# Optimization experiments

Hardware: AMD Instinct MI355X
Metric: run time of the kernel (lower is better)

## Reference

```python
import jax, jax.numpy as jnp
import numpy as np

N = 8192
IN_F = 512
OUT_F = 256

def setup_inputs() -> dict:
    key = jax.random.key(0)
    k1, k2, k3 = jax.random.split(key, 3)
    A = jax.random.uniform(k1, (N, N), dtype=jnp.float32)
    X = jax.random.normal(k2, (N, IN_F), dtype=jnp.float32)
    init_range = np.sqrt(6.0 / (IN_F + OUT_F)).astype(np.float32)
    W = jax.random.uniform(k3, (IN_F, OUT_F), dtype=jnp.float32,
                           minval=-init_range, maxval=init_range)
    return {"weighted_adjacency_matrix": A, "feature_matrix": X, "weight": W}

def reference(weighted_adjacency_matrix, feature_matrix, weight):
    A = weighted_adjacency_matrix
    # d = (1 + row_sum(A))^{-1/2}; D^{-1/2} A D^{-1/2} via row/col broadcast scaling
    d = jax.lax.rsqrt(1.0 + jnp.sum(A, axis=1))            # [N]
    norm_adj = d[:, None] * A * d[None, :]                  # [N, N]
    support = feature_matrix @ weight                       # [N, out_features]
    return norm_adj @ support                               # [N, out_features]
```

## Files before the change

### kernel.cpp

```cpp
#include <hip/hip_runtime.h>
#include <hip/hip_bf16.h>
#include <stdint.h>

#define NROW 8192
#define INF  512
#define OUTF 256

typedef __attribute__((ext_vector_type(8))) short bf16x8;
typedef __attribute__((ext_vector_type(4))) float f32x4;

__device__ __forceinline__ unsigned short f2bf(float x) {
  union { float f; unsigned u; } v; v.f = x;
  unsigned r = v.u + 0x7fffu + ((v.u >> 16) & 1u);
  return (unsigned short)(r >> 16);
}
__device__ __forceinline__ unsigned short f2bf_fast(float x) {
  union { float f; unsigned u; } v; v.f = x;
  return (unsigned short)((v.u + 0x8000u) >> 16);
}
__device__ __forceinline__ float bf2f(unsigned short h) {
  union { unsigned u; float f; } v; v.u = ((unsigned)h) << 16;
  return v.f;
}

__device__ __forceinline__ void async_cp16(const void* g, void* l) {
  __builtin_amdgcn_global_load_lds((const __attribute__((address_space(1))) void*)g,
                                   (__attribute__((address_space(3))) void*)l,
                                   16, 0, 0);
}

__global__ __launch_bounds__(256) void k_rowsum_convert(
    const float* __restrict__ A, unsigned short* __restrict__ Ab,
    float* __restrict__ dv) {
  int w = threadIdx.x >> 6, lane = threadIdx.x & 63;
  int row = blockIdx.x * 4 + w;
  const float4* ar = (const float4*)(A + (size_t)row * NROW);
  ushort4* br = (ushort4*)(Ab + (size_t)row * NROW);
  float s = 0.f;
  #pragma unroll 4
  for (int it = 0; it < NROW / 256; ++it) {
    float4 v = ar[it * 64 + lane];
    s += (v.x + v.y) + (v.z + v.w);
    ushort4 b;
    b.x = f2bf_fast(v.x); b.y = f2bf_fast(v.y);
    b.z = f2bf_fast(v.z); b.w = f2bf_fast(v.w);
    br[it * 64 + lane] = b;
  }
  #pragma unroll
  for (int off = 32; off > 0; off >>= 1) s += __shfl_down(s, off, 64);
  if (lane == 0) dv[row] = rsqrtf(1.f + s);
}

__global__ __launch_bounds__(256) void k_convert_w(
    const float* __restrict__ W, unsigned short* __restrict__ WsT) {
  int idx = blockIdx.x * 256 + threadIdx.x;
  int k = idx >> 8, f = idx & 255;
  WsT[(size_t)f * INF + k] = f2bf(W[idx]);
}

__global__ __launch_bounds__(256, 2) void k_support_fx(
    const unsigned short* __restrict__ WsT,
    const float* __restrict__ X,
    const float* __restrict__ dv,
    unsigned short* __restrict__ YT) {
  __shared__ unsigned short lA[128 * 64];
  __shared__ unsigned short lB[128 * 64];
  const int t = threadIdx.x;
  const int w = t >> 6, lane = t & 63;
  const int m0 = blockIdx.x * 128;
  const int n0 = blockIdx.y * 128;
  const int rsub = lane >> 3, csub = lane & 7, swz = csub ^ rsub;
  const int lr = lane & 15, lq = lane >> 4, x7 = lane & 7;
  const int mw = (w >> 1) * 64, nw = (w & 1) * 64;

  const int xrow = t >> 1, xhalf = t & 1;
  const float4* xsrc = (const float4*)(X + (size_t)(n0 + xrow) * INF + xhalf * 32);

  f32x4 acc[4][4];
  #pragma unroll
  for (int i = 0; i < 4; ++i)
    #pragma unroll
    for (int j = 0; j < 4; ++j) acc[i][j] = f32x4{0.f, 0.f, 0.f, 0.f};

  const unsigned short* ga0 = WsT + (size_t)(m0 + w * 8 + rsub) * INF + swz * 8;

  for (int it = 0; it < INF / 64; ++it) {
    __syncthreads();
    #pragma unroll
    for (int i = 0; i < 4; ++i)
      async_cp16(ga0 + (size_t)(i * 32) * INF + it * 64, &lA[(i * 32 + w * 8) * 64]);
    #pragma unroll
    for (int u = 0; u < 8; ++u) {
      float4 v = xsrc[it * 16 + u];
      ushort4 b;
      b.x = f2bf(v.x); b.y = f2bf(v.y); b.z = f2bf(v.z); b.w = f2bf(v.w);
      int k = xhalf * 32 + u * 4;
      int chunk = k >> 3, klo = k & 7;
      int slot = chunk ^ (xrow & 7);
      *(ushort4*)&lB[xrow * 64 + (slot << 3) + klo] = b;
    }
    __syncthreads();
    #pragma unroll
    for (int ks = 0; ks < 2; ++ks) {
      bf16x8 af[4], bfv[4];
      #pragma unroll
      for (int mi = 0; mi < 4; ++mi)
        af[mi] = *(const bf16x8*)&lA[(mw + mi * 16 + lr) * 64 + (((ks * 4 + lq) ^ x7) << 3)];
      #pragma unroll
      for (int ni = 0; ni < 4; ++ni)
        bfv[ni] = *(const bf16x8*)&lB[(nw + ni * 16 + lr) * 64 + (((ks * 4 + lq) ^ x7) << 3)];
      #pragma unroll
      for (int mi = 0; mi < 4; ++mi)
        #pragma unroll
        for (int ni = 0; ni < 4; ++ni)
          acc[mi][ni] = __builtin_amdgcn_mfma_f32_16x16x32_bf16(
              af[mi], bfv[ni], acc[mi][ni], 0, 0, 0);
    }
  }
  #pragma unroll
  for (int mi = 0; mi < 4; ++mi) {
    #pragma unroll
    for (int ni = 0; ni < 4; ++ni) {
      f32x4 a = acc[mi][ni];
      int gr0 = m0 + mw + mi * 16 + lq * 4;
      int gc  = n0 + nw + ni * 16 + lr;
      float dd = dv[gc];
      #pragma unroll
      for (int r = 0; r < 4; ++r)
        YT[(size_t)(gr0 + r) * NROW + gc] = f2bf(dd * a[r]);
    }
  }
}

__global__ __launch_bounds__(256, 2) void k_gemm_main(
    const unsigned short* __restrict__ Ab,
    const unsigned short* __restrict__ YT,
    unsigned short* __restrict__ P) {
  __shared__ unsigned short lA[128 * 64];
  __shared__ unsigned short lB[256 * 64];
  const int t = threadIdx.x;
  const int w = t >> 6, lane = t & 63;
  const int m0 = blockIdx.x * 128;
  const int kz = blockIdx.y * 1024;
  const int rsub = lane >> 3, csub = lane & 7, swz = csub ^ rsub;
  const int lr = lane & 15, lq = lane >> 4, x7 = lane & 7;
  const int mw = (w & 1) * 64;
  const int nw = (w >> 1) * 128;

  f32x4 acc[4][8];
  #pragma unroll
  for (int i = 0; i < 4; ++i)
    #pragma unroll
    for (int j = 0; j < 8; ++j) acc[i][j] = f32x4{0.f, 0.f, 0.f, 0.f};

  const unsigned short* ga0 = Ab + (size_t)(m0 + w * 8 + rsub) * NROW + kz + swz * 8;
  const unsigned short* gb0 = YT + (size_t)(w * 8 + rsub) * NROW + kz + swz * 8;

  for (int it = 0; it < 16; ++it) {
    __syncthreads();
    #pragma unroll
    for (int i = 0; i < 4; ++i)
      async_cp16(ga0 + (size_t)(i * 32) * NROW + it * 64, &lA[(i * 32 + w * 8) * 64]);
    #pragma unroll
    for (int i = 0; i < 8; ++i)
      async_cp16(gb0 + (size_t)(i * 32) * NROW + it * 64, &lB[(i * 32 + w * 8) * 64]);
    __syncthreads();
    #pragma unroll
    for (int ks = 0; ks < 2; ++ks) {
      bf16x8 af[4], bfv[8];
      #pragma unroll
      for (int mi = 0; mi < 4; ++mi)
        af[mi] = *(const bf16x8*)&lA[(mw + mi * 16 + lr) * 64 + (((ks * 4 + lq) ^ x7) << 3)];
      #pragma unroll
      for (int ni = 0; ni < 8; ++ni)
        bfv[ni] = *(const bf16x8*)&lB[(nw + ni * 16 + lr) * 64 + (((ks * 4 + lq) ^ x7) << 3)];
      #pragma unroll
      for (int mi = 0; mi < 4; ++mi)
        #pragma unroll
        for (int ni = 0; ni < 8; ++ni)
          acc[mi][ni] = __builtin_amdgcn_mfma_f32_16x16x32_bf16(
              af[mi], bfv[ni], acc[mi][ni], 0, 0, 0);
    }
  }

  unsigned short* Pz = P + (size_t)blockIdx.y * NROW * OUTF;
  #pragma unroll
  for (int mi = 0; mi < 4; ++mi) {
    #pragma unroll
    for (int ni = 0; ni < 8; ++ni) {
      f32x4 a = acc[mi][ni];
      int gr0 = m0 + mw + mi * 16 + lq * 4;
      int gc  = nw + ni * 16 + lr;
      #pragma unroll
      for (int r = 0; r < 4; ++r)
        Pz[(size_t)(gr0 + r) * OUTF + gc] = f2bf_fast(a[r]);
    }
  }
}

__global__ __launch_bounds__(256) void k_reduce8(
    const ushort4* __restrict__ P4, const float* __restrict__ dv,
    float4* __restrict__ o4) {
  int q = blockIdx.x * 256 + threadIdx.x;
  const int QT = NROW * OUTF / 4;
  float4 s = {0.f, 0.f, 0.f, 0.f};
  #pragma unroll
  for (int z = 0; z < 8; ++z) {
    ushort4 v = P4[(size_t)z * QT + q];
    s.x += bf2f(v.x); s.y += bf2f(v.y); s.z += bf2f(v.z); s.w += bf2f(v.w);
  }
  float dd = dv[q >> 6];
  s.x *= dd; s.y *= dd; s.z *= dd; s.w *= dd;
  o4[q] = s;
}

__global__ __launch_bounds__(256) void k_rowsum_only(
    const float* __restrict__ A, float* __restrict__ dv) {
  int w = threadIdx.x >> 6, lane = threadIdx.x & 63;
  int row = blockIdx.x * 4 + w;
  const float4* ar = (const float4*)(A + (size_t)row * NROW);
  float s = 0.f;
  for (int it = 0; it < NROW / 256; ++it) {
    float4 v = ar[it * 64 + lane];
    s += (v.x + v.y) + (v.z + v.w);
  }
  #pragma unroll
  for (int off = 32; off > 0; off >>= 1) s += __shfl_down(s, off, 64);
  if (lane == 0) dv[row] = rsqrtf(1.f + s);
}

__global__ __launch_bounds__(256) void k_support_naive(
    const float* __restrict__ X, const float* __restrict__ W,
    const float* __restrict__ dv, float* __restrict__ Y) {
  __shared__ float lX[INF];
  int i = blockIdx.x;
  for (int k = threadIdx.x; k < INF; k += 256) lX[k] = X[(size_t)i * INF + k];
  __syncthreads();
  int f = threadIdx.x;
  float s = 0.f;
  for (int k = 0; k < INF; ++k) s += lX[k] * W[(size_t)k * OUTF + f];
  Y[(size_t)i * OUTF + f] = dv[i] * s;
}

__global__ __launch_bounds__(256) void k_main_naive(
    const float* __restrict__ A, const float* __restrict__ Y,
    const float* __restrict__ dv, float* __restrict__ out) {
  __shared__ float lA[256];
  int i = blockIdx.x, f = threadIdx.x;
  float s = 0.f;
  for (int jb = 0; jb < NROW; jb += 256) {
    __syncthreads();
    lA[threadIdx.x] = A[(size_t)i * NROW + jb + threadIdx.x];
    __syncthreads();
    for (int jj = 0; jj < 256; ++jj) s += lA[jj] * Y[(size_t)(jb + jj) * OUTF + f];
  }
  out[(size_t)i * OUTF + f] = dv[i] * s;
}

extern "C" void kernel_launch(void* const* d_in, const int* in_sizes, int n_in,
                              void* d_out, int out_size, void* d_ws, size_t ws_size,
                              hipStream_t stream) {
  const float* A = (const float*)d_in[0];
  const float* X = (const float*)d_in[1];
  const float* W = (const float*)d_in[2];
  float* out = (float*)d_out;

  const size_t SZ_AB  = (size_t)NROW * NROW * 2;
  const size_t SZ_YT  = (size_t)OUTF * NROW * 2;
  const size_t SZ_WST = (size_t)OUTF * INF * 2;
  const size_t SZ_D   = (size_t)NROW * 4;
  const size_t SZ_P   = (size_t)8 * NROW * OUTF * 2;
  const size_t NEED = SZ_AB + SZ_YT + SZ_WST + SZ_D + SZ_P;

  char* p = (char*)d_ws;
  if (ws_size >= NEED) {
    unsigned short* Ab  = (unsigned short*)p; p += SZ_AB;
    unsigned short* YT  = (unsigned short*)p; p += SZ_YT;
    unsigned short* WsT = (unsigned short*)p; p += SZ_WST;
    float* dv = (float*)p; p += SZ_D;
    unsigned short* P = (unsigned short*)p;

    k_rowsum_convert<<<dim3(2048), dim3(256), 0, stream>>>(A, Ab, dv);
    k_convert_w<<<dim3(512), dim3(256), 0, stream>>>(W, WsT);
    k_support_fx<<<dim3(2, 64), dim3(256), 0, stream>>>(WsT, X, dv, YT);
    k_gemm_main<<<dim3(64, 8), dim3(256), 0, stream>>>(Ab, YT, P);
    k_reduce8<<<dim3(2048), dim3(256), 0, stream>>>((const ushort4*)P, dv, (float4*)out);
  } else {
    float* dv = (float*)p; p += SZ_D;
    float* Y  = (float*)p;
    k_rowsum_only<<<dim3(2048), dim3(256), 0, stream>>>(A, dv);
    k_support_naive<<<dim3(8192), dim3(256), 0, stream>>>(X, W, dv, Y);
    k_main_naive<<<dim3(8192), dim3(256), 0, stream>>>(A, Y, dv, out);
  }
}
```

Measured before the change: 457.4 us.

## Fuse fp32-to-bf16 conversion of A into the main GEMM tile load

```diff
diff --git a/kernel.cpp b/kernel.cpp
--- a/kernel.cpp
+++ b/kernel.cpp
@@ -29,22 +29,16 @@
                                    16, 0, 0);
 }
 
-__global__ __launch_bounds__(256) void k_rowsum_convert(
-    const float* __restrict__ A, unsigned short* __restrict__ Ab,
-    float* __restrict__ dv) {
+__global__ __launch_bounds__(256) void k_rowsum(
+    const float* __restrict__ A, float* __restrict__ dv) {
   int w = threadIdx.x >> 6, lane = threadIdx.x & 63;
   int row = blockIdx.x * 4 + w;
   const float4* ar = (const float4*)(A + (size_t)row * NROW);
-  ushort4* br = (ushort4*)(Ab + (size_t)row * NROW);
   float s = 0.f;
   #pragma unroll 4
   for (int it = 0; it < NROW / 256; ++it) {
     float4 v = ar[it * 64 + lane];
     s += (v.x + v.y) + (v.z + v.w);
-    ushort4 b;
-    b.x = f2bf_fast(v.x); b.y = f2bf_fast(v.y);
-    b.z = f2bf_fast(v.z); b.w = f2bf_fast(v.w);
-    br[it * 64 + lane] = b;
   }
   #pragma unroll
   for (int off = 32; off > 0; off >>= 1) s += __shfl_down(s, off, 64);
@@ -132,8 +126,8 @@
   }
 }
 
-__global__ __launch_bounds__(256, 2) void k_gemm_main(
-    const unsigned short* __restrict__ Ab,
+__global__ __launch_bounds__(256, 2) void k_gemm_main_f32a(
+    const float* __restrict__ A,
     const unsigned short* __restrict__ YT,
     unsigned short* __restrict__ P) {
   __shared__ unsigned short lA[128 * 64];
@@ -147,23 +141,37 @@
   const int mw = (w & 1) * 64;
   const int nw = (w >> 1) * 128;
 
+  const int arow = t >> 2, aq = t & 3;
+  const int aklo = (aq & 1) * 4;
+
   f32x4 acc[4][8];
   #pragma unroll
   for (int i = 0; i < 4; ++i)
     #pragma unroll
     for (int j = 0; j < 8; ++j) acc[i][j] = f32x4{0.f, 0.f, 0.f, 0.f};
 
-  const unsigned short* ga0 = Ab + (size_t)(m0 + w * 8 + rsub) * NROW + kz + swz * 8;
   const unsigned short* gb0 = YT + (size_t)(w * 8 + rsub) * NROW + kz + swz * 8;
 
   for (int it = 0; it < 16; ++it) {
     __syncthreads();
-    #pragma unroll
-    for (int i = 0; i < 4; ++i)
-      async_cp16(ga0 + (size_t)(i * 32) * NROW + it * 64, &lA[(i * 32 + w * 8) * 64]);
     #pragma unroll
     for (int i = 0; i < 8; ++i)
       async_cp16(gb0 + (size_t)(i * 32) * NROW + it * 64, &lB[(i * 32 + w * 8) * 64]);
+    #pragma unroll
+    for (int h = 0; h < 2; ++h) {
+      int r = arow + h * 64;
+      const float4* asrc = (const float4*)(A + (size_t)(m0 + r) * NROW + kz + it * 64);
+      #pragma unroll
+      for (int j = 0; j < 4; ++j) {
+        float4 v = asrc[aq + 4 * j];
+        ushort4 b;
+        b.x = f2bf_fast(v.x); b.y = f2bf_fast(v.y);
+        b.z = f2bf_fast(v.z); b.w = f2bf_fast(v.w);
+        int chunk = (aq + 4 * j) >> 1;
+        int slot = chunk ^ (r & 7);
+        *(ushort4*)&lA[r * 64 + (slot << 3) + aklo] = b;
+      }
+    }
     __syncthreads();
     #pragma unroll
     for (int ks = 0; ks < 2; ++ks) {
@@ -212,21 +220,6 @@
   float dd = dv[q >> 6];
   s.x *= dd; s.y *= dd; s.z *= dd; s.w *= dd;
   o4[q] = s;
-}
-
-__global__ __launch_bounds__(256) void k_rowsum_only(
-    const float* __restrict__ A, float* __restrict__ dv) {
-  int w = threadIdx.x >> 6, lane = threadIdx.x & 63;
-  int row = blockIdx.x * 4 + w;
-  const float4* ar = (const float4*)(A + (size_t)row * NROW);
-  float s = 0.f;
-  for (int it = 0; it < NROW / 256; ++it) {
-    float4 v = ar[it * 64 + lane];
-    s += (v.x + v.y) + (v.z + v.w);
-  }
-  #pragma unroll
-  for (int off = 32; off > 0; off >>= 1) s += __shfl_down(s, off, 64);
-  if (lane == 0) dv[row] = rsqrtf(1.f + s);
 }
 
 __global__ __launch_bounds__(256) void k_support_naive(
@@ -265,30 +258,28 @@
   const float* W = (const float*)d_in[2];
   float* out = (float*)d_out;
 
-  const size_t SZ_AB  = (size_t)NROW * NROW * 2;
   const size_t SZ_YT  = (size_t)OUTF * NROW * 2;
   const size_t SZ_WST = (size_t)OUTF * INF * 2;
   const size_t SZ_D   = (size_t)NROW * 4;
   const size_t SZ_P   = (size_t)8 * NROW * OUTF * 2;
-  const size_t NEED = SZ_AB + SZ_YT + SZ_WST + SZ_D + SZ_P;
+  const size_t NEED = SZ_YT + SZ_WST + SZ_D + SZ_P;
 
   char* p = (char*)d_ws;
   if (ws_size >= NEED) {
-    unsigned short* Ab  = (unsigned short*)p; p += SZ_AB;
     unsigned short* YT  = (unsigned short*)p; p += SZ_YT;
     unsigned short* WsT = (unsigned short*)p; p += SZ_WST;
     float* dv = (float*)p; p += SZ_D;
     unsigned short* P = (unsigned short*)p;
 
-    k_rowsum_convert<<<dim3(2048), dim3(256), 0, stream>>>(A, Ab, dv);
     k_convert_w<<<dim3(512), dim3(256), 0, stream>>>(W, WsT);
+    k_rowsum<<<dim3(2048), dim3(256), 0, stream>>>(A, dv);
     k_support_fx<<<dim3(2, 64), dim3(256), 0, stream>>>(WsT, X, dv, YT);
-    k_gemm_main<<<dim3(64, 8), dim3(256), 0, stream>>>(Ab, YT, P);
+    k_gemm_main_f32a<<<dim3(64, 8), dim3(256), 0, stream>>>(A, YT, P);
     k_reduce8<<<dim3(2048), dim3(256), 0, stream>>>((const ushort4*)P, dv, (float4*)out);
   } else {
     float* dv = (float*)p; p += SZ_D;
     float* Y  = (float*)p;
-    k_rowsum_only<<<dim3(2048), dim3(256), 0, stream>>>(A, dv);
+    k_rowsum<<<dim3(2048), dim3(256), 0, stream>>>(A, dv);
     k_support_naive<<<dim3(8192), dim3(256), 0, stream>>>(X, W, dv, Y);
     k_main_naive<<<dim3(8192), dim3(256), 0, stream>>>(A, Y, dv, out);
   }
```

Measured after the change: 454.4 us. Within noise of the previous version (-0.7%).
